# Optimization experiments

Hardware: AMD Instinct MI355X
Metric: run time of the kernel (lower is better)

The kernel has to match this reference:

```python
import jax, jax.numpy as jnp
import numpy as np

NUM_HEADS = 12

def setup_inputs() -> dict:
    key = jax.random.key(0)
    ks = jax.random.split(key, 8)
    B, N, C, H, R = 8, 1024, 768, NUM_HEADS, 4
    hd = C // H
    x = jax.random.normal(ks[0], (B, N, C), dtype=jnp.float32)
    Wqkv = jax.random.normal(ks[1], (3 * C, C), dtype=jnp.float32) * (C ** -0.5)
    Wproj = jax.random.normal(ks[2], (C, C), dtype=jnp.float32) * (C ** -0.5)
    bproj = jnp.zeros((C,), dtype=jnp.float32)
    Aq = jax.random.normal(ks[3], (hd, R), dtype=jnp.float32) * (hd ** -0.5)
    Bq = jax.random.normal(ks[4], (R, hd), dtype=jnp.float32) * (R ** -0.5)
    Av = jax.random.normal(ks[5], (hd, R), dtype=jnp.float32) * (hd ** -0.5)
    Bv = jax.random.normal(ks[6], (R, hd), dtype=jnp.float32) * (R ** -0.5)
    return {"x": x, "Wqkv": Wqkv, "Wproj": Wproj, "bproj": bproj,
            "Aq": Aq, "Bq": Bq, "Av": Av, "Bv": Bv}

def reference(x, Wqkv, Wproj, bproj, Aq, Bq, Av, Bv):
    B, N, C = x.shape
    H = NUM_HEADS
    hd = C // H
    scale = hd ** -0.5
    # QKV projection: [B,N,3C] -> [3,B,H,N,hd]
    qkv = (x @ Wqkv.T).reshape(B, N, 3, H, hd).transpose(2, 0, 3, 1, 4)
    q, k, v = qkv[0], qkv[1], qkv[2]
    # LoRA low-rank deltas on Q and V
    q = q + (q @ Aq) @ Bq
    v = v + (v @ Av) @ Bv
    # Attention scores [B,H,N,N]
    attn = jnp.einsum('bhnd,bhmd->bhnm', q, k) * scale
    attn = jax.nn.softmax(attn, axis=-1)
    out = jnp.einsum('bhnm,bhmd->bhnd', attn, v)  # [B,H,N,hd]
    out = out.transpose(0, 2, 1, 3).reshape(B, N, C)
    return out @ Wproj.T + bproj
```

## Files before the change

### kernel.cpp

```cpp
#include <hip/hip_runtime.h>

#define DEV __device__ __forceinline__

typedef _Float16 f16x8 __attribute__((ext_vector_type(8)));
typedef _Float16 f16x4 __attribute__((ext_vector_type(4)));
typedef float f32x4 __attribute__((ext_vector_type(4)));
typedef float f32x16 __attribute__((ext_vector_type(16)));
typedef unsigned int u32x4 __attribute__((ext_vector_type(4)));
typedef unsigned int u32x2 __attribute__((ext_vector_type(2)));

DEV void glds16(const void* g, void* l) {
    __builtin_amdgcn_global_load_lds(
        (const __attribute__((address_space(1))) void*)g,
        (__attribute__((address_space(3))) void*)l, 16, 0, 0);
}

DEV unsigned pkh(float lo, float hi) {
    return __builtin_bit_cast(unsigned, __builtin_amdgcn_cvt_pkrtz(lo, hi));
}

__global__ __launch_bounds__(256) void prep_all(const float* __restrict__ x,
                                                const float* __restrict__ Wqkv,
                                                const float* __restrict__ Wproj,
                                                const float* __restrict__ Aq,
                                                const float* __restrict__ Bq,
                                                const float* __restrict__ Av,
                                                const float* __restrict__ Bv,
                                                _Float16* __restrict__ Xb,
                                                _Float16* __restrict__ Wqkvb,
                                                _Float16* __restrict__ Wprojb) {
    const int blk = blockIdx.x;
    if (blk < 72) {
        const int bx = blk % 24, cy = blk / 24;
        const int sec = bx / 12;
        const int h = bx - sec * 12;
        const float* Am = sec ? Av : Aq;
        const float* Bm = sec ? Bv : Bq;
        const int base = sec ? (1536 + h * 64) : (h * 64);
        const float scale = sec ? 1.0f : (0.125f * 1.4426950408889634f);
        const int c = cy * 256 + threadIdx.x;
        float t0 = 0.f, t1 = 0.f, t2 = 0.f, t3 = 0.f;
        for (int j = 0; j < 64; ++j) {
            const float w = Wqkv[(size_t)(base + j) * 768 + c];
            t0 += Am[j * 4 + 0] * w;
            t1 += Am[j * 4 + 1] * w;
            t2 += Am[j * 4 + 2] * w;
            t3 += Am[j * 4 + 3] * w;
        }
        for (int i = 0; i < 64; ++i) {
            const float w = Wqkv[(size_t)(base + i) * 768 + c];
            const float val = w + t0 * Bm[i] + t1 * Bm[64 + i] + t2 * Bm[128 + i] + t3 * Bm[192 + i];
            Wqkvb[(size_t)(base + i) * 768 + c] = (_Float16)(val * scale);
        }
        return;
    }
    const float* src;
    _Float16* dst;
    int i;
    if (blk < 6216) {
        i = (blk - 72) * 256 + threadIdx.x;
        src = x; dst = Xb;
    } else if (blk < 6792) {
        i = (blk - 6216) * 256 + threadIdx.x;
        src = Wqkv + 589824; dst = Wqkvb + 589824;
    } else {
        i = (blk - 6792) * 256 + threadIdx.x;
        src = Wproj; dst = Wprojb;
    }
    const float4 v = ((const float4*)src)[i];
    f16x4 o = { (_Float16)v.x, (_Float16)v.y, (_Float16)v.z, (_Float16)v.w };
    *(f16x4*)(dst + (size_t)i * 4) = o;
}

template <int EPI, int MF, int GX, int GY>
__global__ __launch_bounds__(256) void gemm_nt(const _Float16* __restrict__ A,
                                               const _Float16* __restrict__ B,
                                               int Kdim, void* __restrict__ Cout,
                                               const float* __restrict__ bias) {
    constexpr int BM = MF * 32;
    constexpr int XB = GX / 8;
    __shared__ __align__(16) _Float16 As[BM * 64];
    __shared__ __align__(16) _Float16 Bs[128 * 64];
    const int tid = threadIdx.x;
    const int lane = tid & 63, wid = tid >> 6;
    const int l15 = lane & 15, l16 = lane >> 4;
    const int id = blockIdx.x;
    const int xcd = id & 7, c = id >> 3;
    const int bx = xcd * XB + (c % XB), by = c / XB;
    const int m0 = bx * BM, n0 = by << 7;
    const int wm = (wid >> 1) * (MF * 16), wn = (wid & 1) << 6;

    auto stage = [&](int k0) {
#pragma unroll
        for (int rr = 0; rr < MF; ++rr) {
            const int slot = (rr << 8) + tid;
            const int row = slot >> 3, sl = slot & 7;
            glds16(A + (size_t)(m0 + row) * Kdim + k0 + ((sl ^ (row & 7)) << 3),
                   (char*)As + (((rr << 8) + (wid << 6)) << 4));
        }
#pragma unroll
        for (int rr = 0; rr < 4; ++rr) {
            const int slot = (rr << 8) + tid;
            const int row = slot >> 3, sl = slot & 7;
            glds16(B + (size_t)(n0 + row) * Kdim + k0 + ((sl ^ (row & 7)) << 3),
                   (char*)Bs + (((rr << 8) + (wid << 6)) << 4));
        }
    };

    f32x4 acc[MF][4];
#pragma unroll
    for (int i = 0; i < MF; ++i)
#pragma unroll
        for (int j = 0; j < 4; ++j) acc[i][j] = (f32x4){0.f, 0.f, 0.f, 0.f};

    stage(0);
    __syncthreads();

    for (int k0 = 0; k0 < Kdim; k0 += 64) {
        f16x8 af[2][MF], bf[2][4];
#pragma unroll
        for (int kh = 0; kh < 2; ++kh) {
#pragma unroll
            for (int i = 0; i < MF; ++i) {
                const int ra = wm + i * 16 + l15;
                af[kh][i] = *(const f16x8*)((const char*)As + ra * 128 +
                                            ((((kh << 2) + l16) ^ (ra & 7)) << 4));
            }
#pragma unroll
            for (int j = 0; j < 4; ++j) {
                const int rb = wn + j * 16 + l15;
                bf[kh][j] = *(const f16x8*)((const char*)Bs + rb * 128 +
                                            ((((kh << 2) + l16) ^ (rb & 7)) << 4));
            }
        }
        __syncthreads();
        if (k0 + 64 < Kdim) stage(k0 + 64);
        __builtin_amdgcn_sched_barrier(0);
#pragma unroll
        for (int kh = 0; kh < 2; ++kh)
#pragma unroll
            for (int i = 0; i < MF; ++i)
#pragma unroll
                for (int j = 0; j < 4; ++j)
                    acc[i][j] = __builtin_amdgcn_mfma_f32_16x16x32_f16(af[kh][i], bf[kh][j],
                                                                       acc[i][j], 0, 0, 0);
        __syncthreads();
    }

    if (EPI == 0) {
        _Float16* qkv = (_Float16*)Cout;
#pragma unroll
        for (int j = 0; j < 4; ++j) {
            const int col = n0 + wn + j * 16 + l15;
            const int which = col / 768;
            const int rem = col - which * 768;
            const int hh = rem >> 6, d = rem & 63;
#pragma unroll
            for (int i = 0; i < MF; ++i) {
                const int rowb = m0 + wm + i * 16 + (l16 << 2);
                const int b = rowb >> 10, n = rowb & 1023;
                const int b12h = b * 12 + hh;
                if (which == 2) {
                    f16x4 pk = { (_Float16)acc[i][j][0], (_Float16)acc[i][j][1],
                                 (_Float16)acc[i][j][2], (_Float16)acc[i][j][3] };
                    *(f16x4*)(qkv + 12582912 +
                              ((((size_t)b12h * 64 + (n >> 4)) * 64 + d) << 4) + (n & 15)) = pk;
                } else if (which == 1) {
                    const size_t hb = 6291456 + ((size_t)b12h << 16);
#pragma unroll
                    for (int r = 0; r < 4; ++r) {
                        const int kv = n + r;
                        const int off = ((((kv >> 5) << 2) + (d >> 4)) << 9) +
                                        ((((kv & 31) << 1) + ((d >> 3) & 1)) << 3) + (d & 7);
                        qkv[hb + off] = (_Float16)acc[i][j][r];
                    }
                } else {
#pragma unroll
                    for (int r = 0; r < 4; ++r)
                        qkv[(((size_t)b12h << 10) + n + r) * 64 + d] = (_Float16)acc[i][j][r];
                }
            }
        }
    } else {
        float* out = (float*)Cout;
#pragma unroll
        for (int j = 0; j < 4; ++j) {
            const int col = n0 + wn + j * 16 + l15;
            const float bv = bias[col];
#pragma unroll
            for (int i = 0; i < MF; ++i)
#pragma unroll
                for (int r = 0; r < 4; ++r) {
                    const int row = m0 + wm + i * 16 + (l16 << 2) + r;
                    out[(size_t)row * 768 + col] = acc[i][j][r] + bv;
                }
        }
    }
}

__global__ __launch_bounds__(512) void attn_kernel(const _Float16* __restrict__ Qg,
                                                   const _Float16* __restrict__ K4g,
                                                   const _Float16* __restrict__ V4g,
                                                   _Float16* __restrict__ AO) {
    __shared__ float lds_o[4][64][32];
    __shared__ float2 lds_ml[4][32];

    const int tid = threadIdx.x, lane = tid & 63, wid = tid >> 6;
    const int l31 = lane & 31, hi = lane >> 5;
    const int wq = wid & 3, kvhalf = wid >> 2;
    const int bh = blockIdx.x;
    const int q = (blockIdx.y << 7) + (wq << 5) + l31;
    const int tbase = kvhalf << 4;
    const _Float16* K4h = K4g + ((size_t)bh << 16);
    const _Float16* V4h = V4g + ((size_t)bh << 16);

    f16x8 qf[4];
#pragma unroll
    for (int kd = 0; kd < 4; ++kd)
        qf[kd] = *(const f16x8*)(Qg + (((size_t)bh << 10) + q) * 64 + kd * 16 + hi * 8);

    f32x16 o0, o1;
#pragma unroll
    for (int j = 0; j < 16; ++j) { o0[j] = 0.f; o1[j] = 0.f; }
    float m_run = -INFINITY, l_run = 0.f;

    f16x8 kf[4], vf[4];
    f32x16 st;

#pragma unroll
    for (int kd = 0; kd < 4; ++kd)
        kf[kd] = *(const f16x8*)(K4h + ((size_t)((tbase << 2) + kd) << 9) +
                                 (((l31 << 1) + hi) << 3));
#pragma unroll
    for (int j = 0; j < 16; ++j) st[j] = 0.f;
#pragma unroll
    for (int kd = 0; kd < 4; ++kd)
        st = __builtin_amdgcn_mfma_f32_32x32x16_f16(kf[kd], qf[kd], st, 0, 0, 0);
#pragma unroll
    for (int kd = 0; kd < 4; ++kd)
        kf[kd] = *(const f16x8*)(K4h + ((size_t)(((tbase + 1) << 2) + kd) << 9) +
                                 (((l31 << 1) + hi) << 3));

#pragma unroll 1
    for (int kt = 0; kt < 16; ++kt) {
        const int tt = tbase + kt;

#pragma unroll
        for (int dh = 0; dh < 2; ++dh)
#pragma unroll
            for (int ks = 0; ks < 2; ++ks)
                vf[dh * 2 + ks] = *(const f16x8*)(V4h + ((size_t)((tt << 1) + ks) << 10) +
                                                  ((dh * 32 + l31) << 4) + hi * 8);

        const float g0 = fmaxf(fmaxf(st[0], st[1]), st[2]);
        const float g1 = fmaxf(fmaxf(st[3], st[4]), st[5]);
        const float g2 = fmaxf(fmaxf(st[6], st[7]), st[8]);
        const float g3 = fmaxf(fmaxf(st[9], st[10]), st[11]);
        const float g4 = fmaxf(fmaxf(st[12], st[13]), st[14]);
        const float mx = fmaxf(fmaxf(fmaxf(g0, g1), g2), fmaxf(fmaxf(g3, g4), st[15]));
        if (!__all(mx <= m_run + 8.f)) {
            const float mx2 = fmaxf(mx, __shfl_xor(mx, 32));
            const float mnew = fmaxf(m_run, mx2);
            const float fac = __builtin_amdgcn_exp2f(m_run - mnew);
            l_run *= fac;
#pragma unroll
            for (int j = 0; j < 16; ++j) { o0[j] *= fac; o1[j] *= fac; }
            m_run = mnew;
        }
#pragma unroll
        for (int j = 0; j < 16; ++j) st[j] = __builtin_amdgcn_exp2f(st[j] - m_run);
        float sr[8];
#pragma unroll
        for (int j = 0; j < 8; ++j) sr[j] = st[2 * j] + st[2 * j + 1];
#pragma unroll
        for (int j = 0; j < 4; ++j) sr[j] = sr[j] + sr[j + 4];
        l_run += (sr[0] + sr[2]) + (sr[1] + sr[3]);

        const unsigned a0 = pkh(st[0], st[1]),   a1 = pkh(st[2], st[3]);
        const unsigned a2 = pkh(st[4], st[5]),   a3 = pkh(st[6], st[7]);
        const unsigned a4 = pkh(st[8], st[9]),   a5 = pkh(st[10], st[11]);
        const unsigned a6 = pkh(st[12], st[13]), a7 = pkh(st[14], st[15]);
        const unsigned s0 = (unsigned)__shfl_xor((int)(hi ? a0 : a2), 32);
        const unsigned s1 = (unsigned)__shfl_xor((int)(hi ? a1 : a3), 32);
        const unsigned s2 = (unsigned)__shfl_xor((int)(hi ? a4 : a6), 32);
        const unsigned s3 = (unsigned)__shfl_xor((int)(hi ? a5 : a7), 32);

#pragma unroll
        for (int j = 0; j < 16; ++j) st[j] = 0.f;
        __builtin_amdgcn_s_setprio(1);
#pragma unroll
        for (int kd = 0; kd < 4; ++kd)
            st = __builtin_amdgcn_mfma_f32_32x32x16_f16(kf[kd], qf[kd], st, 0, 0, 0);
        __builtin_amdgcn_s_setprio(0);

        const int tn = tbase + ((kt + 2) & 15);
#pragma unroll
        for (int kd = 0; kd < 4; ++kd)
            kf[kd] = *(const f16x8*)(K4h + ((size_t)((tn << 2) + kd) << 9) +
                                     (((l31 << 1) + hi) << 3));
        __builtin_amdgcn_sched_barrier(0);

        const u32x4 w0 = { hi ? s0 : a0, hi ? s1 : a1, hi ? a2 : s0, hi ? a3 : s1 };
        const u32x4 w1 = { hi ? s2 : a4, hi ? s3 : a5, hi ? a6 : s2, hi ? a7 : s3 };
        const f16x8 pa0 = __builtin_bit_cast(f16x8, w0);
        const f16x8 pa1 = __builtin_bit_cast(f16x8, w1);

        __builtin_amdgcn_s_setprio(1);
        o0 = __builtin_amdgcn_mfma_f32_32x32x16_f16(vf[0], pa0, o0, 0, 0, 0);
        o0 = __builtin_amdgcn_mfma_f32_32x32x16_f16(vf[1], pa1, o0, 0, 0, 0);
        o1 = __builtin_amdgcn_mfma_f32_32x32x16_f16(vf[2], pa0, o1, 0, 0, 0);
        o1 = __builtin_amdgcn_mfma_f32_32x32x16_f16(vf[3], pa1, o1, 0, 0, 0);
        __builtin_amdgcn_s_setprio(0);
    }

    l_run += __shfl_xor(l_run, 32);

    if (kvhalf) {
#pragma unroll
        for (int g = 0; g < 4; ++g) {
            *(f32x4*)&lds_o[wq][lane][4 * g] =
                (f32x4){o0[4 * g + 0], o0[4 * g + 1], o0[4 * g + 2], o0[4 * g + 3]};
            *(f32x4*)&lds_o[wq][lane][16 + 4 * g] =
                (f32x4){o1[4 * g + 0], o1[4 * g + 1], o1[4 * g + 2], o1[4 * g + 3]};
        }
        if (!hi) lds_ml[wq][l31] = make_float2(m_run, l_run);
    }
    __syncthreads();
    if (kvhalf) return;

    const float2 ml2 = lds_ml[wq][l31];
    const float M = fmaxf(m_run, ml2.x);
    const float f1 = __builtin_amdgcn_exp2f(m_run - M);
    const float f2 = __builtin_amdgcn_exp2f(ml2.x - M);
    const float inv = __builtin_amdgcn_rcpf(l_run * f1 + ml2.y * f2);
    const float c1 = f1 * inv, c2 = f2 * inv;

    const int b = bh / 12, h = bh - (bh / 12) * 12;
    _Float16* dst = AO + ((size_t)b * 1024 + q) * 768 + h * 64 + hi * 4;
#pragma unroll
    for (int g = 0; g < 4; ++g) {
        const f32x4 p0 = *(const f32x4*)&lds_o[wq][lane][4 * g];
        const f32x4 p1 = *(const f32x4*)&lds_o[wq][lane][16 + 4 * g];
        const u32x2 w0 = { pkh(o0[4 * g + 0] * c1 + p0[0] * c2, o0[4 * g + 1] * c1 + p0[1] * c2),
                           pkh(o0[4 * g + 2] * c1 + p0[2] * c2, o0[4 * g + 3] * c1 + p0[3] * c2) };
        *(f16x4*)(dst + g * 8) = __builtin_bit_cast(f16x4, w0);
        const u32x2 w1 = { pkh(o1[4 * g + 0] * c1 + p1[0] * c2, o1[4 * g + 1] * c1 + p1[1] * c2),
                           pkh(o1[4 * g + 2] * c1 + p1[2] * c2, o1[4 * g + 3] * c1 + p1[3] * c2) };
        *(f16x4*)(dst + 32 + g * 8) = __builtin_bit_cast(f16x4, w1);
    }
}

extern "C" void kernel_launch(void* const* d_in, const int* in_sizes, int n_in,
                              void* d_out, int out_size, void* d_ws, size_t ws_size,
                              hipStream_t stream) {
    (void)in_sizes; (void)n_in; (void)out_size; (void)ws_size;
    const float* x     = (const float*)d_in[0];
    const float* Wqkv  = (const float*)d_in[1];
    const float* Wproj = (const float*)d_in[2];
    const float* bproj = (const float*)d_in[3];
    const float* Aq    = (const float*)d_in[4];
    const float* Bq    = (const float*)d_in[5];
    const float* Av    = (const float*)d_in[6];
    const float* Bv    = (const float*)d_in[7];

    _Float16* Xb     = (_Float16*)d_ws;
    _Float16* Wqkvb  = Xb + 6291456;
    _Float16* Wprojb = Wqkvb + 1769472;
    _Float16* QKV    = Wprojb + 589824;
    _Float16* AO     = QKV + 18874368;
    float* out = (float*)d_out;

    prep_all<<<7368, 256, 0, stream>>>(x, Wqkv, Wproj, Aq, Bq, Av, Bv,
                                       Xb, Wqkvb, Wprojb);

    gemm_nt<0, 4, 64, 18><<<1152, 256, 0, stream>>>(Xb, Wqkvb, 768, (void*)QKV, nullptr);
    attn_kernel<<<dim3(96, 8), 512, 0, stream>>>(QKV, QKV + 6291456, QKV + 12582912, AO);
    gemm_nt<1, 2, 128, 6><<<768, 256, 0, stream>>>(AO, Wprojb, 768, (void*)out, bproj);
}
```

Before: 114.7 us.

## Store GEMM A operands in MFMA-fragment tiled layout and double-buffer B in LDS

The prep kernel and the attention epilogue now write X and the attention output in a 16-row by 8-column tiled layout. This lets both GEMMs load A fragments straight from global memory into registers without going through LDS. The B tile is double-buffered in LDS, so each K step needs one barrier instead of two and the next B tile loads while MFMAs run. The cost is direct global A loads, which rely on L2/cache hits, and scattered 8-byte writes in the attention epilogue.

```diff
diff --git a/kernel.cpp b/kernel.cpp
--- a/kernel.cpp
+++ b/kernel.cpp
@@ -26,7 +26,7 @@
                                                 const float* __restrict__ Bq,
                                                 const float* __restrict__ Av,
                                                 const float* __restrict__ Bv,
-                                                _Float16* __restrict__ Xb,
+                                                _Float16* __restrict__ Xb4,
                                                 _Float16* __restrict__ Wqkvb,
                                                 _Float16* __restrict__ Wprojb) {
     const int blk = blockIdx.x;
@@ -54,13 +54,19 @@
         }
         return;
     }
+    if (blk < 6216) {
+        const int i4 = (blk - 72) * 256 + threadIdx.x;
+        const int row = i4 / 192, k = (i4 - row * 192) * 4;
+        const float4 v = ((const float4*)x)[i4];
+        f16x4 o = { (_Float16)v.x, (_Float16)v.y, (_Float16)v.z, (_Float16)v.w };
+        *(f16x4*)(Xb4 + (((size_t)(row >> 4) * 96 + (k >> 3)) << 7) +
+                  ((row & 15) << 3) + (k & 7)) = o;
+        return;
+    }
     const float* src;
     _Float16* dst;
     int i;
-    if (blk < 6216) {
-        i = (blk - 72) * 256 + threadIdx.x;
-        src = x; dst = Xb;
-    } else if (blk < 6792) {
+    if (blk < 6792) {
         i = (blk - 6216) * 256 + threadIdx.x;
         src = Wqkv + 589824; dst = Wqkvb + 589824;
     } else {
@@ -73,14 +79,14 @@
 }
 
 template <int EPI, int MF, int GX, int GY>
-__global__ __launch_bounds__(256) void gemm_nt(const _Float16* __restrict__ A,
-                                               const _Float16* __restrict__ B,
-                                               int Kdim, void* __restrict__ Cout,
-                                               const float* __restrict__ bias) {
+__global__ __launch_bounds__(256) void gemm_nt2(const _Float16* __restrict__ A4,
+                                                const _Float16* __restrict__ B,
+                                                void* __restrict__ Cout,
+                                                const float* __restrict__ bias) {
+    constexpr int KD = 768, KS = 96;
     constexpr int BM = MF * 32;
     constexpr int XB = GX / 8;
-    __shared__ __align__(16) _Float16 As[BM * 64];
-    __shared__ __align__(16) _Float16 Bs[128 * 64];
+    __shared__ __align__(16) _Float16 Bs[2][128 * 64];
     const int tid = threadIdx.x;
     const int lane = tid & 63, wid = tid >> 6;
     const int l15 = lane & 15, l16 = lane >> 4;
@@ -89,21 +95,15 @@
     const int bx = xcd * XB + (c % XB), by = c / XB;
     const int m0 = bx * BM, n0 = by << 7;
     const int wm = (wid >> 1) * (MF * 16), wn = (wid & 1) << 6;
-
-    auto stage = [&](int k0) {
-#pragma unroll
-        for (int rr = 0; rr < MF; ++rr) {
-            const int slot = (rr << 8) + tid;
-            const int row = slot >> 3, sl = slot & 7;
-            glds16(A + (size_t)(m0 + row) * Kdim + k0 + ((sl ^ (row & 7)) << 3),
-                   (char*)As + (((rr << 8) + (wid << 6)) << 4));
-        }
+    const int mt0 = (m0 + wm) >> 4;
+
+    auto stageB = [&](int half, int k0) {
 #pragma unroll
         for (int rr = 0; rr < 4; ++rr) {
             const int slot = (rr << 8) + tid;
             const int row = slot >> 3, sl = slot & 7;
-            glds16(B + (size_t)(n0 + row) * Kdim + k0 + ((sl ^ (row & 7)) << 3),
-                   (char*)Bs + (((rr << 8) + (wid << 6)) << 4));
+            glds16(B + (size_t)(n0 + row) * KD + k0 + ((sl ^ (row & 7)) << 3),
+                   (char*)&Bs[half][0] + (((rr << 8) + (wid << 6)) << 4));
         }
     };
 
@@ -113,37 +113,40 @@
 #pragma unroll
         for (int j = 0; j < 4; ++j) acc[i][j] = (f32x4){0.f, 0.f, 0.f, 0.f};
 
-    stage(0);
+    stageB(0, 0);
     __syncthreads();
 
-    for (int k0 = 0; k0 < Kdim; k0 += 64) {
-        f16x8 af[2][MF], bf[2][4];
+    int half = 0;
+#pragma unroll 1
+    for (int k0 = 0; k0 < KD; k0 += 64) {
+        f16x8 af[2][MF];
+#pragma unroll
+        for (int kh = 0; kh < 2; ++kh)
+#pragma unroll
+            for (int i = 0; i < MF; ++i)
+                af[kh][i] = *(const f16x8*)(A4 +
+                    ((size_t)((mt0 + i) * KS + (k0 >> 3) + (kh << 2) + l16) << 7) +
+                    (l15 << 3));
+        __builtin_amdgcn_sched_barrier(0);
+        if (k0 + 64 < KD) stageB(half ^ 1, k0 + 64);
+        __builtin_amdgcn_sched_barrier(0);
 #pragma unroll
         for (int kh = 0; kh < 2; ++kh) {
-#pragma unroll
-            for (int i = 0; i < MF; ++i) {
-                const int ra = wm + i * 16 + l15;
-                af[kh][i] = *(const f16x8*)((const char*)As + ra * 128 +
-                                            ((((kh << 2) + l16) ^ (ra & 7)) << 4));
-            }
+            f16x8 bf[4];
 #pragma unroll
             for (int j = 0; j < 4; ++j) {
                 const int rb = wn + j * 16 + l15;
-                bf[kh][j] = *(const f16x8*)((const char*)Bs + rb * 128 +
-                                            ((((kh << 2) + l16) ^ (rb & 7)) << 4));
+                bf[j] = *(const f16x8*)((const char*)&Bs[half][0] + rb * 128 +
+                                        ((((kh << 2) + l16) ^ (rb & 7)) << 4));
             }
-        }
-        __syncthreads();
-        if (k0 + 64 < Kdim) stage(k0 + 64);
-        __builtin_amdgcn_sched_barrier(0);
-#pragma unroll
-        for (int kh = 0; kh < 2; ++kh)
 #pragma unroll
             for (int i = 0; i < MF; ++i)
 #pragma unroll
                 for (int j = 0; j < 4; ++j)
-                    acc[i][j] = __builtin_amdgcn_mfma_f32_16x16x32_f16(af[kh][i], bf[kh][j],
+                    acc[i][j] = __builtin_amdgcn_mfma_f32_16x16x32_f16(af[kh][i], bf[j],
                                                                        acc[i][j], 0, 0, 0);
+        }
+        half ^= 1;
         __syncthreads();
     }
 
@@ -201,7 +204,7 @@
 __global__ __launch_bounds__(512) void attn_kernel(const _Float16* __restrict__ Qg,
                                                    const _Float16* __restrict__ K4g,
                                                    const _Float16* __restrict__ V4g,
-                                                   _Float16* __restrict__ AO) {
+                                                   _Float16* __restrict__ AO4) {
     __shared__ float lds_o[4][64][32];
     __shared__ float2 lds_ml[4][32];
 
@@ -335,18 +338,18 @@
     const float inv = __builtin_amdgcn_rcpf(l_run * f1 + ml2.y * f2);
     const float c1 = f1 * inv, c2 = f2 * inv;
 
-    const int b = bh / 12, h = bh - (bh / 12) * 12;
-    _Float16* dst = AO + ((size_t)b * 1024 + q) * 768 + h * 64 + hi * 4;
+    const int b = bh / 12, h = bh - b * 12;
+    _Float16* dst = AO4 + (((size_t)(b * 64 + (q >> 4)) * 96) << 7) + ((q & 15) << 3) + hi * 4;
 #pragma unroll
     for (int g = 0; g < 4; ++g) {
         const f32x4 p0 = *(const f32x4*)&lds_o[wq][lane][4 * g];
         const f32x4 p1 = *(const f32x4*)&lds_o[wq][lane][16 + 4 * g];
         const u32x2 w0 = { pkh(o0[4 * g + 0] * c1 + p0[0] * c2, o0[4 * g + 1] * c1 + p0[1] * c2),
                            pkh(o0[4 * g + 2] * c1 + p0[2] * c2, o0[4 * g + 3] * c1 + p0[3] * c2) };
-        *(f16x4*)(dst + g * 8) = __builtin_bit_cast(f16x4, w0);
+        *(f16x4*)(dst + ((size_t)(h * 8 + g) << 7)) = __builtin_bit_cast(f16x4, w0);
         const u32x2 w1 = { pkh(o1[4 * g + 0] * c1 + p1[0] * c2, o1[4 * g + 1] * c1 + p1[1] * c2),
                            pkh(o1[4 * g + 2] * c1 + p1[2] * c2, o1[4 * g + 3] * c1 + p1[3] * c2) };
-        *(f16x4*)(dst + 32 + g * 8) = __builtin_bit_cast(f16x4, w1);
+        *(f16x4*)(dst + ((size_t)(h * 8 + 4 + g) << 7)) = __builtin_bit_cast(f16x4, w1);
     }
 }
 
@@ -363,17 +366,17 @@
     const float* Av    = (const float*)d_in[6];
     const float* Bv    = (const float*)d_in[7];
 
-    _Float16* Xb     = (_Float16*)d_ws;
-    _Float16* Wqkvb  = Xb + 6291456;
+    _Float16* Xb4    = (_Float16*)d_ws;
+    _Float16* Wqkvb  = Xb4 + 6291456;
     _Float16* Wprojb = Wqkvb + 1769472;
     _Float16* QKV    = Wprojb + 589824;
-    _Float16* AO     = QKV + 18874368;
+    _Float16* AO4    = QKV + 18874368;
     float* out = (float*)d_out;
 
     prep_all<<<7368, 256, 0, stream>>>(x, Wqkv, Wproj, Aq, Bq, Av, Bv,
-                                       Xb, Wqkvb, Wprojb);
-
-    gemm_nt<0, 4, 64, 18><<<1152, 256, 0, stream>>>(Xb, Wqkvb, 768, (void*)QKV, nullptr);
-    attn_kernel<<<dim3(96, 8), 512, 0, stream>>>(QKV, QKV + 6291456, QKV + 12582912, AO);
-    gemm_nt<1, 2, 128, 6><<<768, 256, 0, stream>>>(AO, Wprojb, 768, (void*)out, bproj);
-}
+                                       Xb4, Wqkvb, Wprojb);
+
+    gemm_nt2<0, 4, 64, 18><<<1152, 256, 0, stream>>>(Xb4, Wqkvb, (void*)QKV, nullptr);
+    attn_kernel<<<dim3(96, 8), 512, 0, stream>>>(QKV, QKV + 6291456, QKV + 12582912, AO4);
+    gemm_nt2<1, 2, 128, 6><<<768, 256, 0, stream>>>(AO4, Wprojb, (void*)out, bproj);
+}
```

New measurement: 124.8 us (median of 2 runs). 8.9% more time.
